# Performance work log

Hardware: AMD Instinct MI355X
Metric: run time of the kernel (lower is better)

The kernel has to match this reference:

```python
import jax, jax.numpy as jnp
import numpy as np
import math

B, S, HID, NH = 4, 256, 512, 8
D = HID // NH


def setup_inputs() -> dict:
    key = jax.random.key(0)
    ks = jax.random.split(key, 12)
    inp = {
        "q_hidden_states": jax.random.normal(ks[0], (B, S, HID), dtype=jnp.float32),
        "k_hidden_states": jax.random.normal(ks[1], (B, S, HID), dtype=jnp.float32),
        "v_hidden_states": jax.random.normal(ks[2], (B, S, HID), dtype=jnp.float32),
        "Wq": jax.random.normal(ks[3], (HID, HID), dtype=jnp.float32) * 0.02,
        "bq": jnp.zeros((HID,), dtype=jnp.float32),
        "Wk": jax.random.normal(ks[4], (HID, HID), dtype=jnp.float32) * 0.02,
        "bk": jnp.zeros((HID,), dtype=jnp.float32),
        "Wv": jax.random.normal(ks[5], (HID, HID), dtype=jnp.float32) * 0.02,
        "bv": jnp.zeros((HID,), dtype=jnp.float32),
        "rel_table": (jax.random.normal(ks[6], (8, HID), dtype=jnp.float32) * 0.02).at[0].set(0.0),  # padding_idx=0
        "edge_type": jax.random.randint(ks[7], (B, S, S), 0, 8, dtype=jnp.int32),
        "trans_mask": jax.random.randint(ks[8], (B, S, S), 0, 2, dtype=jnp.int32),
    }
    return inp


def _split_heads(x):
    # [B, S, HID] -> [B, NH, S, D]
    b, s, _ = x.shape
    return x.reshape(b, s, NH, D).transpose(0, 2, 1, 3)


def reference(q_hidden_states, k_hidden_states, v_hidden_states,
              Wq, bq, Wk, bk, Wv, bv, rel_table, edge_type, trans_mask):
    scale = 1.0 / math.sqrt(D)
    Q0 = _split_heads(q_hidden_states @ Wq + bq)  # [B,H,S,D]
    K0 = _split_heads(k_hidden_states @ Wk + bk)
    V0 = _split_heads(v_hidden_states @ Wv + bv)

    # Faithful vectorization of the torch loop:
    # at iteration i, Q and K have accumulated sum_{t<=i} rel_layer_t, and only
    # row i of the full QK^T is kept. Hence:
    #   scores[b,h,i,j] = (Q0[i] + C[i,i]) . (K0[j] + C[i,j]) / sqrt(D)
    # where C[t,p] = cumsum over t of rel_emb[:, t, p].
    R = rel_table[edge_type]                                  # [B,S,S,HID]
    C = jnp.cumsum(R.reshape(B, S, S, NH, D), axis=1)         # [B,t,p,H,D]
    idx = jnp.arange(S)
    diagC = C[:, idx, idx].transpose(0, 2, 1, 3)              # [B,H,S,D]: C[:,i,i]
    qrow = Q0 + diagC                                         # [B,H,S,D]

    scores = (jnp.einsum('bhid,bhjd->bhij', qrow, K0)
              + jnp.einsum('bhid,bijhd->bhij', qrow, C)) * scale

    scores = jnp.where(trans_mask[:, None, :, :] == 0, -1e9, scores)
    probs = jax.nn.softmax(scores, axis=-1)  # dropout omitted (eval mode)

    ctx = jnp.einsum('bhij,bhjd->bhid', probs, V0)            # [B,H,S,D]
    return ctx.transpose(0, 2, 1, 3).reshape(B, S, HID)
```

## Files before the change

### kernel.cpp

```cpp
#include <hip/hip_runtime.h>
#include <math.h>

#define BB 4
#define SS 256
#define HID 512
#define NHD 8
#define DD 64
#define IT 16

typedef __attribute__((ext_vector_type(8))) short short8v;
typedef __attribute__((ext_vector_type(4))) float f32x4;

static __device__ __forceinline__ ushort f2bf(float x) {
    uint u = __float_as_uint(x);
    uint r = u + 0x7fffu + ((u >> 16) & 1u);
    return (ushort)(r >> 16);
}
static __device__ __forceinline__ float bf2f(ushort h) {
    return __uint_as_float(((uint)h) << 16);
}
static __device__ __forceinline__ void cvt8(const float4& a, const float4& b,
                                            short8v& hi, short8v& lo) {
    ushort h;
    h = f2bf(a.x); hi[0] = (short)h; lo[0] = (short)f2bf(a.x - bf2f(h));
    h = f2bf(a.y); hi[1] = (short)h; lo[1] = (short)f2bf(a.y - bf2f(h));
    h = f2bf(a.z); hi[2] = (short)h; lo[2] = (short)f2bf(a.z - bf2f(h));
    h = f2bf(a.w); hi[3] = (short)h; lo[3] = (short)f2bf(a.w - bf2f(h));
    h = f2bf(b.x); hi[4] = (short)h; lo[4] = (short)f2bf(b.x - bf2f(h));
    h = f2bf(b.y); hi[5] = (short)h; lo[5] = (short)f2bf(b.y - bf2f(h));
    h = f2bf(b.z); hi[6] = (short)h; lo[6] = (short)f2bf(b.z - bf2f(h));
    h = f2bf(b.w); hi[7] = (short)h; lo[7] = (short)f2bf(b.w - bf2f(h));
}

__global__ __launch_bounds__(256) void prep_kernel(
    const int* __restrict__ edge, uint4* __restrict__ cnt,
    const float* __restrict__ wq, const float* __restrict__ wk, const float* __restrict__ wv,
    ushort* __restrict__ Whi, ushort* __restrict__ Wlo)
{
    __shared__ float tile[32][33];
    const int bid = blockIdx.x;
    const int t = threadIdx.x;

    if (bid < 256) {
        const int wave = t >> 6, lane = t & 63;
        const int col = bid * 4 + wave;
        const int b = col / SS, j = col % SS;

        uint4 run = make_uint4(0, 0, 0, 0);
        uint4 c[4];
        #pragma unroll
        for (int r = 0; r < 4; ++r) {
            const int e = edge[((size_t)(b * SS + lane * 4 + r)) * SS + j];
            const unsigned inc = 1u << ((e & 1) * 16);
            const int comp = e >> 1;
            run.x += (comp == 0) ? inc : 0u;
            run.y += (comp == 1) ? inc : 0u;
            run.z += (comp == 2) ? inc : 0u;
            run.w += (comp == 3) ? inc : 0u;
            c[r] = run;
        }
        uint4 tot = run;
        #pragma unroll
        for (int off = 1; off < 64; off <<= 1) {
            uint4 s;
            s.x = __shfl_up((int)tot.x, off);
            s.y = __shfl_up((int)tot.y, off);
            s.z = __shfl_up((int)tot.z, off);
            s.w = __shfl_up((int)tot.w, off);
            if (lane >= off) { tot.x += s.x; tot.y += s.y; tot.z += s.z; tot.w += s.w; }
        }
        const uint4 excl = make_uint4(tot.x - run.x, tot.y - run.y, tot.z - run.z, tot.w - run.w);
        #pragma unroll
        for (int r = 0; r < 4; ++r) {
            uint4 o = make_uint4(excl.x + c[r].x, excl.y + c[r].y, excl.z + c[r].z, excl.w + c[r].w);
            cnt[((size_t)(b * SS + lane * 4 + r)) * SS + j] = o;
        }
    } else {
        const int v = bid - 256;
        const int bx = v & 15, by = (v >> 4) & 15, z = v >> 8;
        const float* W = (z == 0) ? wq : (z == 1) ? wk : wv;
        const int k0 = bx * 32, n0 = by * 32;
        {
            const int r = t >> 3, c4 = (t & 7) * 4;
            *(float4*)&tile[r][c4] = *(const float4*)&W[(size_t)(k0 + r) * HID + n0 + c4];
        }
        __syncthreads();
        {
            const int n = t >> 3, kc = (t & 7) * 4;
            ushort4 hi, lo;
            float x;
            x = tile[kc + 0][n]; hi.x = f2bf(x); lo.x = f2bf(x - bf2f(hi.x));
            x = tile[kc + 1][n]; hi.y = f2bf(x); lo.y = f2bf(x - bf2f(hi.y));
            x = tile[kc + 2][n]; hi.z = f2bf(x); lo.z = f2bf(x - bf2f(hi.z));
            x = tile[kc + 3][n]; hi.w = f2bf(x); lo.w = f2bf(x - bf2f(hi.w));
            const size_t o = (size_t)z * (512 * 512) + (size_t)(n0 + n) * HID + k0 + kc;
            *(ushort4*)&Whi[o] = hi;
            *(ushort4*)&Wlo[o] = lo;
        }
    }
}

__global__ __launch_bounds__(256) void qkv_gemm_mfma(
    const float* __restrict__ xq, const float* __restrict__ xk, const float* __restrict__ xv,
    const ushort* __restrict__ Whi, const ushort* __restrict__ Wlo,
    const float* __restrict__ bq, const float* __restrict__ bk, const float* __restrict__ bv,
    float* __restrict__ oq, float* __restrict__ ok, float* __restrict__ ov)
{
    const int z = blockIdx.z;
    const float* X    = (z == 0) ? xq : (z == 1) ? xk : xv;
    const float* bias = (z == 0) ? bq : (z == 1) ? bk : bv;
    float*       out  = (z == 0) ? oq : (z == 1) ? ok : ov;
    const size_t wb = (size_t)z * (512 * 512);

    __shared__ ushort As_hi[64][40];
    __shared__ ushort As_lo[64][40];
    __shared__ ushort Bs_hi[64][40];
    __shared__ ushort Bs_lo[64][40];

    const int t = threadIdx.x;
    const int wave = t >> 6, lane = t & 63;
    const int wr = wave >> 1, wc = wave & 1;
    const int bm = blockIdx.x * 64, bn = blockIdx.y * 64;

    const int sm = t >> 2, sk = (t & 3) * 8;
    const int fr = lane & 15, kb = (lane >> 4) * 8;

    f32x4 acc[2][2] = {};

    for (int k0 = 0; k0 < HID; k0 += 32) {
        {
            const float* xp = &X[(size_t)(bm + sm) * HID + k0 + sk];
            const float4 a0 = *(const float4*)&xp[0];
            const float4 a1 = *(const float4*)&xp[4];
            short8v h8, l8;
            cvt8(a0, a1, h8, l8);
            *(short8v*)&As_hi[sm][sk] = h8;
            *(short8v*)&As_lo[sm][sk] = l8;
        }
        *(uint4*)&Bs_hi[sm][sk] = *(const uint4*)&Whi[wb + (size_t)(bn + sm) * HID + k0 + sk];
        *(uint4*)&Bs_lo[sm][sk] = *(const uint4*)&Wlo[wb + (size_t)(bn + sm) * HID + k0 + sk];
        __syncthreads();

        short8v ah[2], al[2], bh[2], bl[2];
        #pragma unroll
        for (int mi = 0; mi < 2; ++mi) {
            ah[mi] = *(const short8v*)&As_hi[wr * 32 + mi * 16 + fr][kb];
            al[mi] = *(const short8v*)&As_lo[wr * 32 + mi * 16 + fr][kb];
        }
        #pragma unroll
        for (int ni = 0; ni < 2; ++ni) {
            bh[ni] = *(const short8v*)&Bs_hi[wc * 32 + ni * 16 + fr][kb];
            bl[ni] = *(const short8v*)&Bs_lo[wc * 32 + ni * 16 + fr][kb];
        }
        #pragma unroll
        for (int mi = 0; mi < 2; ++mi)
            #pragma unroll
            for (int ni = 0; ni < 2; ++ni) {
                acc[mi][ni] = __builtin_amdgcn_mfma_f32_16x16x32_bf16(ah[mi], bh[ni], acc[mi][ni], 0, 0, 0);
                acc[mi][ni] = __builtin_amdgcn_mfma_f32_16x16x32_bf16(ah[mi], bl[ni], acc[mi][ni], 0, 0, 0);
                acc[mi][ni] = __builtin_amdgcn_mfma_f32_16x16x32_bf16(al[mi], bh[ni], acc[mi][ni], 0, 0, 0);
            }
        __syncthreads();
    }

    const int r0 = bm + wr * 32 + (lane >> 4) * 4;
    const int c0 = bn + wc * 32 + (lane & 15);
    #pragma unroll
    for (int ni = 0; ni < 2; ++ni) {
        const float bia = bias[c0 + ni * 16];
        #pragma unroll
        for (int mi = 0; mi < 2; ++mi)
            #pragma unroll
            for (int q = 0; q < 4; ++q)
                out[(size_t)(r0 + mi * 16 + q) * HID + c0 + ni * 16] = acc[mi][ni][q] + bia;
    }
}

__global__ __launch_bounds__(256) void attn_fused(
    const float* __restrict__ Q0,
    const float* __restrict__ K0,
    const float* __restrict__ V0,
    const float* __restrict__ rel,
    const uint4* __restrict__ cnt,
    const int* __restrict__ mask,
    float* __restrict__ out)
{
    const int x = blockIdx.x;
    const int it = x & 15;
    const int h  = (x >> 4) & 7;
    const int b  = x >> 7;
    const int i0 = it * IT;
    const int t = threadIdx.x, wave = t >> 6, lane = t & 63;

    __shared__ ushort qhi[16][72];
    __shared__ ushort qlo[16][72];
    __shared__ float qre_s[IT][8];
    __shared__ float s_t[SS][20];
    __shared__ float vtile[64][68];

    const int pi = t >> 4, pd = t & 15;
    float4 qr4;
    {
        const float4 q4 = *(const float4*)&Q0[((size_t)(b * SS + i0 + pi)) * HID + h * DD + pd * 4];
        const uint4 cv = cnt[((size_t)(b * SS + i0 + pi)) * SS + (i0 + pi)];
        float c[8];
        c[0] = (float)(cv.x & 0xffff); c[1] = (float)(cv.x >> 16);
        c[2] = (float)(cv.y & 0xffff); c[3] = (float)(cv.y >> 16);
        c[4] = (float)(cv.z & 0xffff); c[5] = (float)(cv.z >> 16);
        c[6] = (float)(cv.w & 0xffff); c[7] = (float)(cv.w >> 16);
        float o0 = q4.x, o1 = q4.y, o2 = q4.z, o3 = q4.w;
        #pragma unroll
        for (int e = 0; e < 8; ++e) {
            const float4 r4 = *(const float4*)&rel[e * HID + h * DD + pd * 4];
            o0 += c[e] * r4.x; o1 += c[e] * r4.y; o2 += c[e] * r4.z; o3 += c[e] * r4.w;
        }
        qr4.x = o0; qr4.y = o1; qr4.z = o2; qr4.w = o3;
        ushort4 h4, l4;
        h4.x = f2bf(o0); l4.x = f2bf(o0 - bf2f(h4.x));
        h4.y = f2bf(o1); l4.y = f2bf(o1 - bf2f(h4.y));
        h4.z = f2bf(o2); l4.z = f2bf(o2 - bf2f(h4.z));
        h4.w = f2bf(o3); l4.w = f2bf(o3 - bf2f(h4.w));
        *(ushort4*)&qhi[pi][pd * 4] = h4;
        *(ushort4*)&qlo[pi][pd * 4] = l4;
    }
    {
        float r[8];
        #pragma unroll
        for (int e = 0; e < 8; ++e) {
            const float4 rr = *(const float4*)&rel[e * HID + h * DD + pd * 4];
            r[e] = qr4.x * rr.x + qr4.y * rr.y + qr4.z * rr.z + qr4.w * rr.w;
        }
        #pragma unroll
        for (int e = 0; e < 8; ++e) {
            float v = r[e];
            v += __shfl_xor(v, 1);
            v += __shfl_xor(v, 2);
            v += __shfl_xor(v, 4);
            v += __shfl_xor(v, 8);
            r[e] = v;
        }
        float sel = 0.f;
        #pragma unroll
        for (int e = 0; e < 8; ++e) if (pd == e) sel = r[e];
        if (pd < 8) qre_s[pi][pd] = sel;
    }
    __syncthreads();

    {
        const int fr = lane & 15, kb8 = (lane >> 4) * 8;
        const int jt = wave;
        const int ib = (lane >> 4) * 4;

        short8v qh[2], ql[2];
        #pragma unroll
        for (int ks = 0; ks < 2; ++ks) {
            qh[ks] = *(const short8v*)&qhi[fr][ks * 32 + kb8];
            ql[ks] = *(const short8v*)&qlo[fr][ks * 32 + kb8];
        }
        float4 qa[4], qb[4];
        #pragma unroll
        for (int q = 0; q < 4; ++q) {
            qa[q] = *(const float4*)&qre_s[ib + q][0];
            qb[q] = *(const float4*)&qre_s[ib + q][4];
        }

        #pragma unroll
        for (int jf = 0; jf < 4; ++jf) {
            const int j = jt * 64 + jf * 16 + fr;
            const float* Kr = &K0[((size_t)(b * SS + j)) * HID + h * DD];
            f32x4 acc = {};
            #pragma unroll
            for (int ks = 0; ks < 2; ++ks) {
                const float4 k0v = *(const float4*)&Kr[ks * 32 + kb8];
                const float4 k1v = *(const float4*)&Kr[ks * 32 + kb8 + 4];
                short8v kh, kl;
                cvt8(k0v, k1v, kh, kl);
                acc = __builtin_amdgcn_mfma_f32_16x16x32_bf16(qh[ks], kh, acc, 0, 0, 0);
                acc = __builtin_amdgcn_mfma_f32_16x16x32_bf16(qh[ks], kl, acc, 0, 0, 0);
                acc = __builtin_amdgcn_mfma_f32_16x16x32_bf16(ql[ks], kh, acc, 0, 0, 0);
            }
            float sv[4];
            #pragma unroll
            for (int q = 0; q < 4; ++q) {
                const int i = ib + q;
                const uint4 cv = cnt[((size_t)(b * SS + i0 + i)) * SS + j];
                float s = acc[q]
                    + qa[q].x * (float)(cv.x & 0xffff) + qa[q].y * (float)(cv.x >> 16)
                    + qa[q].z * (float)(cv.y & 0xffff) + qa[q].w * (float)(cv.y >> 16)
                    + qb[q].x * (float)(cv.z & 0xffff) + qb[q].y * (float)(cv.z >> 16)
                    + qb[q].z * (float)(cv.w & 0xffff) + qb[q].w * (float)(cv.w >> 16);
                s *= 0.125f;
                const int m = mask[((size_t)(b * SS + i0 + i)) * SS + j];
                sv[q] = m ? s : -1e9f;
            }
            float4 w4; w4.x = sv[0]; w4.y = sv[1]; w4.z = sv[2]; w4.w = sv[3];
            *(float4*)&s_t[j][ib] = w4;
        }
    }
    __syncthreads();

    {
        #pragma unroll
        for (int rr = 0; rr < 4; ++rr) {
            const int i = wave * 4 + rr;
            float v0 = s_t[lane][i], v1 = s_t[lane + 64][i],
                  v2 = s_t[lane + 128][i], v3 = s_t[lane + 192][i];
            float mx = fmaxf(fmaxf(v0, v1), fmaxf(v2, v3));
            #pragma unroll
            for (int off = 32; off > 0; off >>= 1) mx = fmaxf(mx, __shfl_xor(mx, off));
            float e0 = __expf(v0 - mx), e1 = __expf(v1 - mx),
                  e2 = __expf(v2 - mx), e3 = __expf(v3 - mx);
            float sm = e0 + e1 + e2 + e3;
            #pragma unroll
            for (int off = 32; off > 0; off >>= 1) sm += __shfl_xor(sm, off);
            const float inv = 1.f / sm;
            s_t[lane][i] = e0 * inv;
            s_t[lane + 64][i] = e1 * inv;
            s_t[lane + 128][i] = e2 * inv;
            s_t[lane + 192][i] = e3 * inv;
        }
    }
    __syncthreads();

    {
        const int iq = wave;
        const int jsub = (t >> 4) & 3, dq = t & 15;
        float o[4][4] = {};
        for (int jt = 0; jt < 4; ++jt) {
            {
                const int jr = t >> 2, seg = t & 3;
                const float* src = &V0[((size_t)(b * SS + jt * 64 + jr)) * HID + h * DD + seg * 16];
                #pragma unroll
                for (int qq = 0; qq < 4; ++qq)
                    *(float4*)&vtile[jr][seg * 16 + qq * 4] = *(const float4*)&src[qq * 4];
            }
            __syncthreads();
            #pragma unroll
            for (int jj = 0; jj < 16; ++jj) {
                const int j = jsub * 16 + jj;
                const float4 p4 = *(const float4*)&s_t[jt * 64 + j][iq * 4];
                const float4 v4 = *(const float4*)&vtile[j][dq * 4];
                o[0][0] += p4.x * v4.x; o[0][1] += p4.x * v4.y;
                o[0][2] += p4.x * v4.z; o[0][3] += p4.x * v4.w;
                o[1][0] += p4.y * v4.x; o[1][1] += p4.y * v4.y;
                o[1][2] += p4.y * v4.z; o[1][3] += p4.y * v4.w;
                o[2][0] += p4.z * v4.x; o[2][1] += p4.z * v4.y;
                o[2][2] += p4.z * v4.z; o[2][3] += p4.z * v4.w;
                o[3][0] += p4.w * v4.x; o[3][1] += p4.w * v4.y;
                o[3][2] += p4.w * v4.z; o[3][3] += p4.w * v4.w;
            }
            __syncthreads();
        }
        #pragma unroll
        for (int r = 0; r < 4; ++r)
            #pragma unroll
            for (int c = 0; c < 4; ++c) {
                float v = o[r][c];
                v += __shfl_xor(v, 16);
                v += __shfl_xor(v, 32);
                o[r][c] = v;
            }
        float sel0 = 0.f, sel1 = 0.f, sel2 = 0.f, sel3 = 0.f;
        #pragma unroll
        for (int r = 0; r < 4; ++r)
            if (r == jsub) { sel0 = o[r][0]; sel1 = o[r][1]; sel2 = o[r][2]; sel3 = o[r][3]; }
        const int i = iq * 4 + jsub;
        float4 ov; ov.x = sel0; ov.y = sel1; ov.z = sel2; ov.w = sel3;
        *(float4*)&out[((size_t)(b * SS + i0 + i)) * HID + h * DD + dq * 4] = ov;
    }
}

extern "C" void kernel_launch(void* const* d_in, const int* in_sizes, int n_in,
                              void* d_out, int out_size, void* d_ws, size_t ws_size,
                              hipStream_t stream) {
    const float* q_hs = (const float*)d_in[0];
    const float* k_hs = (const float*)d_in[1];
    const float* v_hs = (const float*)d_in[2];
    const float* Wq   = (const float*)d_in[3];
    const float* bq   = (const float*)d_in[4];
    const float* Wk   = (const float*)d_in[5];
    const float* bk   = (const float*)d_in[6];
    const float* Wv   = (const float*)d_in[7];
    const float* bv   = (const float*)d_in[8];
    const float* rel  = (const float*)d_in[9];
    const int* edge   = (const int*)d_in[10];
    const int* mask   = (const int*)d_in[11];
    float* out = (float*)d_out;

    char* ws = (char*)d_ws;
    float*  Q    = (float*)(ws);
    float*  K0   = (float*)(ws + (2u  << 20));
    float*  V0   = (float*)(ws + (4u  << 20));
    uint4*  cnt  = (uint4*)(ws + (6u  << 20));
    ushort* Wthi = (ushort*)(ws + (10u << 20));
    ushort* Wtlo = (ushort*)(ws + (12u << 20));

    prep_kernel<<<dim3(1024), 256, 0, stream>>>(edge, cnt, Wq, Wk, Wv, Wthi, Wtlo);
    {
        dim3 grid(1024 / 64, HID / 64, 3);
        qkv_gemm_mfma<<<grid, 256, 0, stream>>>(q_hs, k_hs, v_hs, Wthi, Wtlo,
                                                bq, bk, bv, Q, K0, V0);
    }
    attn_fused<<<dim3(BB * NHD * (SS / IT)), 256, 0, stream>>>(Q, K0, V0, rel, cnt, mask, out);
}
```

Baseline: 117.7 us.

## Fuse weight split into QKV GEMM and merge count-scan into same launch

```diff
diff --git a/kernel.cpp b/kernel.cpp
--- a/kernel.cpp
+++ b/kernel.cpp
@@ -32,20 +32,20 @@
     h = f2bf(b.w); hi[7] = (short)h; lo[7] = (short)f2bf(b.w - bf2f(h));
 }
 
-__global__ __launch_bounds__(256) void prep_kernel(
-    const int* __restrict__ edge, uint4* __restrict__ cnt,
+__global__ __launch_bounds__(256) void gemm_cnt(
+    const float* __restrict__ xq, const float* __restrict__ xk, const float* __restrict__ xv,
     const float* __restrict__ wq, const float* __restrict__ wk, const float* __restrict__ wv,
-    ushort* __restrict__ Whi, ushort* __restrict__ Wlo)
+    const float* __restrict__ bq, const float* __restrict__ bk, const float* __restrict__ bv,
+    float* __restrict__ oq, float* __restrict__ ok, float* __restrict__ ov,
+    const int* __restrict__ edge, uint4* __restrict__ cnt)
 {
-    __shared__ float tile[32][33];
     const int bid = blockIdx.x;
     const int t = threadIdx.x;
-
-    if (bid < 256) {
-        const int wave = t >> 6, lane = t & 63;
-        const int col = bid * 4 + wave;
+    const int wave = t >> 6, lane = t & 63;
+
+    if (bid >= 384) {
+        const int col = (bid - 384) * 4 + wave;
         const int b = col / SS, j = col % SS;
-
         uint4 run = make_uint4(0, 0, 0, 0);
         uint4 c[4];
         #pragma unroll
@@ -75,54 +75,24 @@
             uint4 o = make_uint4(excl.x + c[r].x, excl.y + c[r].y, excl.z + c[r].z, excl.w + c[r].w);
             cnt[((size_t)(b * SS + lane * 4 + r)) * SS + j] = o;
         }
-    } else {
-        const int v = bid - 256;
-        const int bx = v & 15, by = (v >> 4) & 15, z = v >> 8;
-        const float* W = (z == 0) ? wq : (z == 1) ? wk : wv;
-        const int k0 = bx * 32, n0 = by * 32;
-        {
-            const int r = t >> 3, c4 = (t & 7) * 4;
-            *(float4*)&tile[r][c4] = *(const float4*)&W[(size_t)(k0 + r) * HID + n0 + c4];
-        }
-        __syncthreads();
-        {
-            const int n = t >> 3, kc = (t & 7) * 4;
-            ushort4 hi, lo;
-            float x;
-            x = tile[kc + 0][n]; hi.x = f2bf(x); lo.x = f2bf(x - bf2f(hi.x));
-            x = tile[kc + 1][n]; hi.y = f2bf(x); lo.y = f2bf(x - bf2f(hi.y));
-            x = tile[kc + 2][n]; hi.z = f2bf(x); lo.z = f2bf(x - bf2f(hi.z));
-            x = tile[kc + 3][n]; hi.w = f2bf(x); lo.w = f2bf(x - bf2f(hi.w));
-            const size_t o = (size_t)z * (512 * 512) + (size_t)(n0 + n) * HID + k0 + kc;
-            *(ushort4*)&Whi[o] = hi;
-            *(ushort4*)&Wlo[o] = lo;
-        }
-    }
-}
-
-__global__ __launch_bounds__(256) void qkv_gemm_mfma(
-    const float* __restrict__ xq, const float* __restrict__ xk, const float* __restrict__ xv,
-    const ushort* __restrict__ Whi, const ushort* __restrict__ Wlo,
-    const float* __restrict__ bq, const float* __restrict__ bk, const float* __restrict__ bv,
-    float* __restrict__ oq, float* __restrict__ ok, float* __restrict__ ov)
-{
-    const int z = blockIdx.z;
-    const float* X    = (z == 0) ? xq : (z == 1) ? xk : xv;
-    const float* bias = (z == 0) ? bq : (z == 1) ? bk : bv;
-    float*       out  = (z == 0) ? oq : (z == 1) ? ok : ov;
-    const size_t wb = (size_t)z * (512 * 512);
+        return;
+    }
 
     __shared__ ushort As_hi[64][40];
     __shared__ ushort As_lo[64][40];
     __shared__ ushort Bs_hi[64][40];
     __shared__ ushort Bs_lo[64][40];
 
-    const int t = threadIdx.x;
-    const int wave = t >> 6, lane = t & 63;
+    const int z = bid / 128, rr = bid % 128;
+    const float* X    = (z == 0) ? xq : (z == 1) ? xk : xv;
+    const float* W    = (z == 0) ? wq : (z == 1) ? wk : wv;
+    const float* bias = (z == 0) ? bq : (z == 1) ? bk : bv;
+    float*       out  = (z == 0) ? oq : (z == 1) ? ok : ov;
+    const int bm = (rr & 15) * 64, bn = (rr >> 4) * 64;
+
     const int wr = wave >> 1, wc = wave & 1;
-    const int bm = blockIdx.x * 64, bn = blockIdx.y * 64;
-
     const int sm = t >> 2, sk = (t & 3) * 8;
+    const int wn = t & 63, wks = (t >> 6) * 8;
     const int fr = lane & 15, kb = (lane >> 4) * 8;
 
     f32x4 acc[2][2] = {};
@@ -137,8 +107,21 @@
             *(short8v*)&As_hi[sm][sk] = h8;
             *(short8v*)&As_lo[sm][sk] = l8;
         }
-        *(uint4*)&Bs_hi[sm][sk] = *(const uint4*)&Whi[wb + (size_t)(bn + sm) * HID + k0 + sk];
-        *(uint4*)&Bs_lo[sm][sk] = *(const uint4*)&Wlo[wb + (size_t)(bn + sm) * HID + k0 + sk];
+        {
+            float wv8[8];
+            #pragma unroll
+            for (int j = 0; j < 8; ++j)
+                wv8[j] = W[(size_t)(k0 + wks + j) * HID + bn + wn];
+            short8v wh, wl;
+            #pragma unroll
+            for (int j = 0; j < 8; ++j) {
+                const ushort h = f2bf(wv8[j]);
+                wh[j] = (short)h;
+                wl[j] = (short)f2bf(wv8[j] - bf2f(h));
+            }
+            *(short8v*)&Bs_hi[wn][wks] = wh;
+            *(short8v*)&Bs_lo[wn][wks] = wl;
+        }
         __syncthreads();
 
         short8v ah[2], al[2], bh[2], bl[2];
@@ -392,14 +375,8 @@
     float*  K0   = (float*)(ws + (2u  << 20));
     float*  V0   = (float*)(ws + (4u  << 20));
     uint4*  cnt  = (uint4*)(ws + (6u  << 20));
-    ushort* Wthi = (ushort*)(ws + (10u << 20));
-    ushort* Wtlo = (ushort*)(ws + (12u << 20));
-
-    prep_kernel<<<dim3(1024), 256, 0, stream>>>(edge, cnt, Wq, Wk, Wv, Wthi, Wtlo);
-    {
-        dim3 grid(1024 / 64, HID / 64, 3);
-        qkv_gemm_mfma<<<grid, 256, 0, stream>>>(q_hs, k_hs, v_hs, Wthi, Wtlo,
-                                                bq, bk, bv, Q, K0, V0);
-    }
+
+    gemm_cnt<<<dim3(640), 256, 0, stream>>>(q_hs, k_hs, v_hs, Wq, Wk, Wv,
+                                            bq, bk, bv, Q, K0, V0, edge, cnt);
     attn_fused<<<dim3(BB * NHD * (SS / IT)), 256, 0, stream>>>(Q, K0, V0, rel, cnt, mask, out);
 }
```

After: 113.1 us. -3.9%, faster.
